# Kernel tuning notes

Measured on AMD Instinct MI355X. Metric: run time of the kernel, lower is better.

The kernel has to match this reference:

```python
import jax, jax.numpy as jnp
import numpy as np

H = 4096          # hidden_size
I = 2048          # moe_intermediate_size * n_shared_experts
SWIGLU_LIMIT = 10.0
QMAX = 127.0


def _quantize_weight(w):
    # per-output-channel symmetric int8 quantization of a float weight [out, in]
    s = jnp.maximum(jnp.max(jnp.abs(w), axis=1) / QMAX, 1e-8)      # [out]
    q = jnp.clip(jnp.round(w / s[:, None]), -QMAX, QMAX)           # int8-valued
    return q.astype(jnp.float32), s.astype(jnp.float32)


def setup_inputs() -> dict:
    key = jax.random.key(0)
    ks = jax.random.split(key, 4)
    x = jax.random.normal(ks[0], (2, 4096, H), dtype=jnp.float32)
    w_gate, s_wgate = _quantize_weight(jax.random.normal(ks[1], (I, H)) * 0.02)
    w_up, s_wup = _quantize_weight(jax.random.normal(ks[2], (I, H)) * 0.02)
    w_down, s_wdown = _quantize_weight(jax.random.normal(ks[3], (H, I)) * 0.02)
    inv_gate = jnp.ones((H,), jnp.float32)
    inv_up = jnp.ones((H,), jnp.float32)
    inv_inter = jnp.ones((I,), jnp.float32)
    return {"x": x, "w_gate": w_gate, "s_wgate": s_wgate, "w_up": w_up,
            "s_wup": s_wup, "w_down": w_down, "s_wdown": s_wdown,
            "inv_gate": inv_gate, "inv_up": inv_up, "inv_inter": inv_inter}


def _dynamic_quant(x, inv_smooth):
    # per-token symmetric int8 dynamic quant with smoothing scale
    xs = x.astype(jnp.float32) * inv_smooth                        # [T, D]
    scale = jnp.maximum(jnp.max(jnp.abs(xs), axis=-1, keepdims=True) / QMAX, 1e-8)
    q = jnp.clip(jnp.round(xs / scale), -QMAX, QMAX)
    return q, scale


def _quant_gemm(q, x_scale, w_q, w_scale):
    acc = q @ w_q.T                                                # fp32 accumulate
    return acc * x_scale * w_scale[None, :]


def reference(x, w_gate, s_wgate, w_up, s_wup, w_down, s_wdown,
              inv_gate, inv_up, inv_inter):
    orig_shape = x.shape
    x_flat = x.reshape(-1, H).astype(jnp.bfloat16)                 # [T, H]
    qg, sg = _dynamic_quant(x_flat, inv_gate)
    qu, su = _dynamic_quant(x_flat, inv_up)
    gate_out = _quant_gemm(qg, sg, w_gate, s_wgate)                # [T, I]
    up_out = _quant_gemm(qu, su, w_up, s_wup)                      # [T, I]
    inter = jax.nn.silu(gate_out) * up_out
    inter = jnp.clip(inter, -SWIGLU_LIMIT, SWIGLU_LIMIT).astype(jnp.bfloat16)
    qi, si = _dynamic_quant(inter, inv_inter)
    out = _quant_gemm(qi, si, w_down, s_wdown)                     # [T, H]
    return out.reshape(orig_shape)
```

## Files before the change

### kernel.cpp

```cpp
#include <hip/hip_runtime.h>
#include <hip/hip_bf16.h>


typedef __attribute__((ext_vector_type(4))) int i32x4;
typedef __attribute__((ext_vector_type(16))) int i32x16;

__device__ __forceinline__ void async16(void* lds, const void* g) {
  __builtin_amdgcn_global_load_lds(
      (const __attribute__((address_space(1))) void*)g,
      (__attribute__((address_space(3))) void*)lds, 16, 0, 0);
}

__device__ __forceinline__ i32x16 mfma32(i32x4 a, i32x4 b, i32x16 c) {
  return __builtin_amdgcn_mfma_i32_32x32x32_i8(a, b, c, 0, 0, 0);
}

__device__ __forceinline__ float bf16_rne_f(float f) {
  unsigned u = __float_as_uint(f);
  u += 0x7fffu + ((u >> 16) & 1u);
  return __uint_as_float(u & 0xffff0000u);
}
__device__ __forceinline__ unsigned short bf16_bits(float f) {
  unsigned u = __float_as_uint(f);
  u += 0x7fffu + ((u >> 16) & 1u);
  return (unsigned short)(u >> 16);
}
__device__ __forceinline__ float bf16_to_f(unsigned short h) {
  return __uint_as_float(((unsigned)h) << 16);
}

__global__ void wconv3_kernel(const float* __restrict__ w0,
                              const float* __restrict__ w1,
                              const float* __restrict__ w2,
                              signed char* __restrict__ q0,
                              signed char* __restrict__ q1,
                              signed char* __restrict__ q2, int n) {
  const float* w = (blockIdx.y == 0) ? w0 : (blockIdx.y == 1) ? w1 : w2;
  signed char* q = (blockIdx.y == 0) ? q0 : (blockIdx.y == 1) ? q1 : q2;
  int i = (blockIdx.x * 256 + threadIdx.x) * 4;
  if (i >= n) return;
  float4 f = *(const float4*)(w + i);
  signed char c[4] __attribute__((aligned(4)));
  c[0] = (signed char)(int)rintf(f.x);
  c[1] = (signed char)(int)rintf(f.y);
  c[2] = (signed char)(int)rintf(f.z);
  c[3] = (signed char)(int)rintf(f.w);
  *(int*)(q + i) = *(const int*)c;
}

__global__ __launch_bounds__(256) void quant_x_kernel(
    const float* __restrict__ x, const float* __restrict__ invg,
    const float* __restrict__ invu, signed char* __restrict__ qg,
    signed char* __restrict__ qu, float* __restrict__ sg,
    float* __restrict__ su, int H) {
  const int t = blockIdx.x, tid = threadIdx.x;
  const float* xr = x + (size_t)t * H;
  const int c0 = tid * 16;
  float xg[16], xu[16];
  float mg = 0.f, mu = 0.f;
#pragma unroll
  for (int v = 0; v < 4; ++v) {
    float4 f = *(const float4*)(xr + c0 + v * 4);
    float4 ig = *(const float4*)(invg + c0 + v * 4);
    float4 iu = *(const float4*)(invu + c0 + v * 4);
    float b0 = bf16_rne_f(f.x), b1 = bf16_rne_f(f.y);
    float b2 = bf16_rne_f(f.z), b3 = bf16_rne_f(f.w);
    xg[v * 4 + 0] = b0 * ig.x; xg[v * 4 + 1] = b1 * ig.y;
    xg[v * 4 + 2] = b2 * ig.z; xg[v * 4 + 3] = b3 * ig.w;
    xu[v * 4 + 0] = b0 * iu.x; xu[v * 4 + 1] = b1 * iu.y;
    xu[v * 4 + 2] = b2 * iu.z; xu[v * 4 + 3] = b3 * iu.w;
#pragma unroll
    for (int j = 0; j < 4; ++j) {
      mg = fmaxf(mg, fabsf(xg[v * 4 + j]));
      mu = fmaxf(mu, fabsf(xu[v * 4 + j]));
    }
  }
#pragma unroll
  for (int off = 32; off > 0; off >>= 1) {
    mg = fmaxf(mg, __shfl_xor(mg, off));
    mu = fmaxf(mu, __shfl_xor(mu, off));
  }
  __shared__ float smg[4], smu[4];
  if ((tid & 63) == 0) { smg[tid >> 6] = mg; smu[tid >> 6] = mu; }
  __syncthreads();
  mg = fmaxf(fmaxf(smg[0], smg[1]), fmaxf(smg[2], smg[3]));
  mu = fmaxf(fmaxf(smu[0], smu[1]), fmaxf(smu[2], smu[3]));
  const float scg = fmaxf(mg / 127.0f, 1e-8f);
  const float scu = fmaxf(mu / 127.0f, 1e-8f);
  const float rg = 1.0f / scg, ru = 1.0f / scu;
  signed char og[16] __attribute__((aligned(16)));
  signed char ou[16] __attribute__((aligned(16)));
#pragma unroll
  for (int j = 0; j < 16; ++j) {
    og[j] = (signed char)(int)fminf(fmaxf(rintf(xg[j] * rg), -127.f), 127.f);
    ou[j] = (signed char)(int)fminf(fmaxf(rintf(xu[j] * ru), -127.f), 127.f);
  }
  *(i32x4*)(qg + (size_t)t * H + c0) = *(const i32x4*)og;
  *(i32x4*)(qu + (size_t)t * H + c0) = *(const i32x4*)ou;
  if (tid == 0) { sg[t] = scg; su[t] = scu; }
}

__global__ __launch_bounds__(256, 2) void gemm1_kernel(
    const signed char* __restrict__ qg, const signed char* __restrict__ qu,
    const float* __restrict__ sg, const float* __restrict__ su,
    const signed char* __restrict__ wg, const signed char* __restrict__ wu,
    const float* __restrict__ swg, const float* __restrict__ swu,
    unsigned short* __restrict__ inter, int H, int I) {
  __shared__ signed char Ag[128 * 64] __attribute__((aligned(16)));
  __shared__ signed char Au[128 * 64] __attribute__((aligned(16)));
  __shared__ signed char Bg[128 * 64] __attribute__((aligned(16)));
  __shared__ signed char Bu[128 * 64] __attribute__((aligned(16)));
  const int tid = threadIdx.x;
  const int lane = tid & 63, wave = tid >> 6;
  const int col0 = blockIdx.x * 128, row0 = blockIdx.y * 128;
  const int wm = (wave & 1) * 64, wn = (wave >> 1) * 64;
  const int m = lane & 31, h = lane >> 5;

  i32x16 accG[2][2], accU[2][2];
#pragma unroll
  for (int i = 0; i < 2; ++i)
#pragma unroll
    for (int j = 0; j < 2; ++j) {
      accG[i][j] = (i32x16)(0);
      accU[i][j] = (i32x16)(0);
    }

  for (int kk = 0; kk < H; kk += 64) {
    __syncthreads();
#pragma unroll
    for (int p = 0; p < 2; ++p) {
      const int g = p * 256 + tid;
      const int r = g >> 2;
      const int cg = ((g & 3) - r) & 3;
      const size_t ga = (size_t)(row0 + r) * H + kk + cg * 16;
      const size_t gb = (size_t)(col0 + r) * H + kk + cg * 16;
      async16(&Ag[g * 16], qg + ga);
      async16(&Au[g * 16], qu + ga);
      async16(&Bg[g * 16], wg + gb);
      async16(&Bu[g * 16], wu + gb);
    }
    __syncthreads();
#pragma unroll
    for (int s = 0; s < 2; ++s) {
      i32x4 aG[2], aU[2], bG[2], bU[2];
#pragma unroll
      for (int i = 0; i < 2; ++i) {
        const int ra = wm + i * 32 + m;
        const int ca = ((s * 2 + h + ra) & 3) * 16;
        aG[i] = *(const i32x4*)&Ag[ra * 64 + ca];
        aU[i] = *(const i32x4*)&Au[ra * 64 + ca];
        const int rb = wn + i * 32 + m;
        const int cb = ((s * 2 + h + rb) & 3) * 16;
        bG[i] = *(const i32x4*)&Bg[rb * 64 + cb];
        bU[i] = *(const i32x4*)&Bu[rb * 64 + cb];
      }
#pragma unroll
      for (int i = 0; i < 2; ++i)
#pragma unroll
        for (int j = 0; j < 2; ++j) {
          accG[i][j] = mfma32(aG[i], bG[j], accG[i][j]);
          accU[i][j] = mfma32(aU[i], bU[j], accU[i][j]);
        }
    }
  }

  float swgc[2], swuc[2];
#pragma unroll
  for (int j = 0; j < 2; ++j) {
    const int c = col0 + wn + j * 32 + m;
    swgc[j] = swg[c];
    swuc[j] = swu[c];
  }
#pragma unroll
  for (int i = 0; i < 2; ++i) {
#pragma unroll
    for (int reg = 0; reg < 16; ++reg) {
      const int row = row0 + wm + i * 32 + (reg & 3) + 8 * (reg >> 2) + 4 * h;
      const float sgr = sg[row], sur = su[row];
#pragma unroll
      for (int j = 0; j < 2; ++j) {
        const int c = col0 + wn + j * 32 + m;
        const float g = (float)accG[i][j][reg] * sgr * swgc[j];
        const float u = (float)accU[i][j][reg] * sur * swuc[j];
        const float sig = 1.f / (1.f + __expf(-g));
        float v = (g * sig) * u;
        v = fminf(fmaxf(v, -10.f), 10.f);
        inter[(size_t)row * I + c] = bf16_bits(v);
      }
    }
  }
}

__global__ __launch_bounds__(256) void quant_i_kernel(
    const unsigned short* __restrict__ inter, const float* __restrict__ invi,
    signed char* __restrict__ qi, float* __restrict__ si, int I) {
  const int t = blockIdx.x, tid = threadIdx.x;
  const unsigned short* ir = inter + (size_t)t * I;
  const int c0 = tid * 8;
  uint4 pk = *(const uint4*)(ir + c0);
  float4 i0 = *(const float4*)(invi + c0);
  float4 i1 = *(const float4*)(invi + c0 + 4);
  float xs[8];
  xs[0] = bf16_to_f(pk.x & 0xffffu) * i0.x;
  xs[1] = bf16_to_f(pk.x >> 16) * i0.y;
  xs[2] = bf16_to_f(pk.y & 0xffffu) * i0.z;
  xs[3] = bf16_to_f(pk.y >> 16) * i0.w;
  xs[4] = bf16_to_f(pk.z & 0xffffu) * i1.x;
  xs[5] = bf16_to_f(pk.z >> 16) * i1.y;
  xs[6] = bf16_to_f(pk.w & 0xffffu) * i1.z;
  xs[7] = bf16_to_f(pk.w >> 16) * i1.w;
  float m = 0.f;
#pragma unroll
  for (int j = 0; j < 8; ++j) m = fmaxf(m, fabsf(xs[j]));
#pragma unroll
  for (int off = 32; off > 0; off >>= 1) m = fmaxf(m, __shfl_xor(m, off));
  __shared__ float sm[4];
  if ((tid & 63) == 0) sm[tid >> 6] = m;
  __syncthreads();
  m = fmaxf(fmaxf(sm[0], sm[1]), fmaxf(sm[2], sm[3]));
  const float s = fmaxf(m / 127.0f, 1e-8f);
  const float rs = 1.0f / s;
  signed char o[8] __attribute__((aligned(8)));
#pragma unroll
  for (int j = 0; j < 8; ++j)
    o[j] = (signed char)(int)fminf(fmaxf(rintf(xs[j] * rs), -127.f), 127.f);
  *(unsigned long long*)(qi + (size_t)t * I + c0) = *(const unsigned long long*)o;
  if (tid == 0) si[t] = s;
}

__global__ __launch_bounds__(256, 2) void gemm2_kernel(
    const signed char* __restrict__ qi, const float* __restrict__ si,
    const signed char* __restrict__ wd, const float* __restrict__ swd,
    float* __restrict__ out, int H, int I) {
  __shared__ signed char As[128 * 64] __attribute__((aligned(16)));
  __shared__ signed char Bs[128 * 64] __attribute__((aligned(16)));
  const int tid = threadIdx.x;
  const int lane = tid & 63, wave = tid >> 6;
  const int col0 = blockIdx.x * 128, row0 = blockIdx.y * 128;
  const int wm = (wave & 1) * 64, wn = (wave >> 1) * 64;
  const int m = lane & 31, h = lane >> 5;

  i32x16 acc[2][2];
#pragma unroll
  for (int i = 0; i < 2; ++i)
#pragma unroll
    for (int j = 0; j < 2; ++j) acc[i][j] = (i32x16)(0);

  for (int kk = 0; kk < I; kk += 64) {
    __syncthreads();
#pragma unroll
    for (int p = 0; p < 2; ++p) {
      const int g = p * 256 + tid;
      const int r = g >> 2;
      const int cg = ((g & 3) - r) & 3;
      async16(&As[g * 16], qi + (size_t)(row0 + r) * I + kk + cg * 16);
      async16(&Bs[g * 16], wd + (size_t)(col0 + r) * I + kk + cg * 16);
    }
    __syncthreads();
#pragma unroll
    for (int s = 0; s < 2; ++s) {
      i32x4 a[2], b[2];
#pragma unroll
      for (int i = 0; i < 2; ++i) {
        const int ra = wm + i * 32 + m;
        const int ca = ((s * 2 + h + ra) & 3) * 16;
        a[i] = *(const i32x4*)&As[ra * 64 + ca];
        const int rb = wn + i * 32 + m;
        const int cb = ((s * 2 + h + rb) & 3) * 16;
        b[i] = *(const i32x4*)&Bs[rb * 64 + cb];
      }
#pragma unroll
      for (int i = 0; i < 2; ++i)
#pragma unroll
        for (int j = 0; j < 2; ++j) acc[i][j] = mfma32(a[i], b[j], acc[i][j]);
    }
  }

  float swc[2];
#pragma unroll
  for (int j = 0; j < 2; ++j) swc[j] = swd[col0 + wn + j * 32 + m];
#pragma unroll
  for (int i = 0; i < 2; ++i) {
#pragma unroll
    for (int reg = 0; reg < 16; ++reg) {
      const int row = row0 + wm + i * 32 + (reg & 3) + 8 * (reg >> 2) + 4 * h;
      const float sir = si[row];
#pragma unroll
      for (int j = 0; j < 2; ++j) {
        const int c = col0 + wn + j * 32 + m;
        out[(size_t)row * H + c] = (float)acc[i][j][reg] * sir * swc[j];
      }
    }
  }
}

extern "C" void kernel_launch(void* const* d_in, const int* in_sizes, int n_in,
                              void* d_out, int out_size, void* d_ws,
                              size_t ws_size, hipStream_t stream) {
  const float* x = (const float*)d_in[0];
  const float* w_gate = (const float*)d_in[1];
  const float* s_wgate = (const float*)d_in[2];
  const float* w_up = (const float*)d_in[3];
  const float* s_wup = (const float*)d_in[4];
  const float* w_down = (const float*)d_in[5];
  const float* s_wdown = (const float*)d_in[6];
  const float* inv_gate = (const float*)d_in[7];
  const float* inv_up = (const float*)d_in[8];
  const float* inv_inter = (const float*)d_in[9];
  float* out = (float*)d_out;

  const int H = in_sizes[6];
  const int I = in_sizes[2];
  const int T = in_sizes[0] / H;

  char* ws = (char*)d_ws;
  size_t off = 0;
  signed char* wqg = (signed char*)(ws + off); off += (size_t)I * H;
  signed char* wqu = (signed char*)(ws + off); off += (size_t)I * H;
  signed char* wqd = (signed char*)(ws + off); off += (size_t)H * I;
  signed char* qg  = (signed char*)(ws + off); off += (size_t)T * H;
  signed char* qu  = (signed char*)(ws + off); off += (size_t)T * H;
  unsigned short* inter = (unsigned short*)(ws + off); off += (size_t)T * I * 2;
  float* sg = (float*)(ws + off); off += (size_t)T * 4;
  float* su = (float*)(ws + off); off += (size_t)T * 4;
  float* si = (float*)(ws + off); off += (size_t)T * 4;
  signed char* qi = qg;

  const int nW = I * H;
  dim3 gw(nW / 1024, 3);
  wconv3_kernel<<<gw, 256, 0, stream>>>(w_gate, w_up, w_down, wqg, wqu, wqd, nW);

  quant_x_kernel<<<T, 256, 0, stream>>>(x, inv_gate, inv_up, qg, qu, sg, su, H);

  dim3 g1(I / 128, T / 128);
  gemm1_kernel<<<g1, 256, 0, stream>>>(qg, qu, sg, su, wqg, wqu, s_wgate,
                                       s_wup, inter, H, I);

  quant_i_kernel<<<T, 256, 0, stream>>>(inter, inv_inter, qi, si, I);

  dim3 g2(H / 128, T / 128);
  gemm2_kernel<<<g2, 256, 0, stream>>>(qi, si, wqd, s_wdown, out, H, I);
}
```

Baseline: 608.2 us.

## Pre-tile int8 operands into MFMA-native blocked layout for contiguous tile loads

The weight conversion and both activation quant kernels now write int8 data in a blocked layout (32-row tiles, 16-byte k-chunks arranged per MFMA fragment). The GEMMs can then fetch each k-tile with contiguous 16-byte async loads and read LDS fragments at fixed offsets, with no swizzle arithmetic. The grid order is swapped so row blocks vary fastest, and quant_i now handles two tokens per block. In exchange, the weight conversion writes strided output, and the layout only works when T, H and I are multiples of 32 and 64.

```diff
diff --git a/kernel.cpp b/kernel.cpp
--- a/kernel.cpp
+++ b/kernel.cpp
@@ -29,23 +29,36 @@
   return __uint_as_float(((unsigned)h) << 16);
 }
 
-__global__ void wconv3_kernel(const float* __restrict__ w0,
-                              const float* __restrict__ w1,
-                              const float* __restrict__ w2,
-                              signed char* __restrict__ q0,
-                              signed char* __restrict__ q1,
-                              signed char* __restrict__ q2, int n) {
-  const float* w = (blockIdx.y == 0) ? w0 : (blockIdx.y == 1) ? w1 : w2;
-  signed char* q = (blockIdx.y == 0) ? q0 : (blockIdx.y == 1) ? q1 : q2;
-  int i = (blockIdx.x * 256 + threadIdx.x) * 4;
-  if (i >= n) return;
-  float4 f = *(const float4*)(w + i);
-  signed char c[4] __attribute__((aligned(4)));
-  c[0] = (signed char)(int)rintf(f.x);
-  c[1] = (signed char)(int)rintf(f.y);
-  c[2] = (signed char)(int)rintf(f.z);
-  c[3] = (signed char)(int)rintf(f.w);
-  *(int*)(q + i) = *(const int*)c;
+__global__ __launch_bounds__(256) void wconv_kernel(
+    const float* __restrict__ w0, const float* __restrict__ w1,
+    const float* __restrict__ w2, signed char* __restrict__ q0,
+    signed char* __restrict__ q1, signed char* __restrict__ q2,
+    int H, int I) {
+  const int wid = blockIdx.y;
+  const float* w = (wid == 0) ? w0 : (wid == 1) ? w1 : w2;
+  signed char* q = (wid == 0) ? q0 : (wid == 1) ? q1 : q2;
+  const int K = (wid == 2) ? I : H;
+  const int R = (wid == 2) ? H : I;
+  const int rt = blockIdx.x;
+  if (rt * 32 >= R) return;
+  const int m = threadIdx.x & 31, sub = threadIdx.x >> 5;
+  const int row = rt * 32 + m;
+  const int nkc = K >> 4;
+  const size_t outTile = (size_t)rt * K * 32 + (size_t)m * 16;
+  for (int kc = sub; kc < nkc; kc += 8) {
+    const float* src = w + (size_t)row * K + kc * 16;
+    signed char c[16] __attribute__((aligned(16)));
+#pragma unroll
+    for (int v = 0; v < 4; ++v) {
+      float4 f = *(const float4*)(src + v * 4);
+      c[v * 4 + 0] = (signed char)(int)rintf(f.x);
+      c[v * 4 + 1] = (signed char)(int)rintf(f.y);
+      c[v * 4 + 2] = (signed char)(int)rintf(f.z);
+      c[v * 4 + 3] = (signed char)(int)rintf(f.w);
+    }
+    *(i32x4*)(q + outTile + (kc >> 2) * 2048 + (kc & 3) * 512) =
+        *(const i32x4*)c;
+  }
 }
 
 __global__ __launch_bounds__(256) void quant_x_kernel(
@@ -95,8 +108,10 @@
     og[j] = (signed char)(int)fminf(fmaxf(rintf(xg[j] * rg), -127.f), 127.f);
     ou[j] = (signed char)(int)fminf(fmaxf(rintf(xu[j] * ru), -127.f), 127.f);
   }
-  *(i32x4*)(qg + (size_t)t * H + c0) = *(const i32x4*)og;
-  *(i32x4*)(qu + (size_t)t * H + c0) = *(const i32x4*)ou;
+  const size_t off8 = (size_t)(t >> 5) * H * 32 + (tid >> 2) * 2048 +
+                      (tid & 3) * 512 + (t & 31) * 16;
+  *(i32x4*)(qg + off8) = *(const i32x4*)og;
+  *(i32x4*)(qu + off8) = *(const i32x4*)ou;
   if (tid == 0) { sg[t] = scg; su[t] = scu; }
 }
 
@@ -112,9 +127,20 @@
   __shared__ signed char Bu[128 * 64] __attribute__((aligned(16)));
   const int tid = threadIdx.x;
   const int lane = tid & 63, wave = tid >> 6;
-  const int col0 = blockIdx.x * 128, row0 = blockIdx.y * 128;
-  const int wm = (wave & 1) * 64, wn = (wave >> 1) * 64;
+  const int row0 = blockIdx.x * 128, col0 = blockIdx.y * 128;
+  const int ah = wave & 1, bh = wave >> 1;
   const int m = lane & 31, h = lane >> 5;
+
+  const size_t rts = (size_t)H * 32;
+  const int o = tid & 127, mt0 = tid >> 7;
+  const size_t aoff = (size_t)(row0 >> 5) * rts + (size_t)mt0 * rts + o * 16;
+  const size_t boff = (size_t)(col0 >> 5) * rts + (size_t)mt0 * rts + o * 16;
+  const signed char* pAg = qg + aoff;
+  const signed char* pAu = qu + aoff;
+  const signed char* pBg = wg + boff;
+  const signed char* pBu = wu + boff;
+  const int lds0 = tid * 16, lds1 = tid * 16 + 4096;
+  const size_t skip = rts * 2;
 
   i32x16 accG[2][2], accU[2][2];
 #pragma unroll
@@ -125,34 +151,32 @@
       accU[i][j] = (i32x16)(0);
     }
 
-  for (int kk = 0; kk < H; kk += 64) {
+  const signed char* aBaseG = &Ag[ah * 4096 + lane * 16];
+  const signed char* aBaseU = &Au[ah * 4096 + lane * 16];
+  const signed char* bBaseG = &Bg[bh * 4096 + lane * 16];
+  const signed char* bBaseU = &Bu[bh * 4096 + lane * 16];
+
+  for (int kt = 0; kt < (H >> 6); ++kt) {
     __syncthreads();
-#pragma unroll
-    for (int p = 0; p < 2; ++p) {
-      const int g = p * 256 + tid;
-      const int r = g >> 2;
-      const int cg = ((g & 3) - r) & 3;
-      const size_t ga = (size_t)(row0 + r) * H + kk + cg * 16;
-      const size_t gb = (size_t)(col0 + r) * H + kk + cg * 16;
-      async16(&Ag[g * 16], qg + ga);
-      async16(&Au[g * 16], qu + ga);
-      async16(&Bg[g * 16], wg + gb);
-      async16(&Bu[g * 16], wu + gb);
-    }
+    async16(&Ag[lds0], pAg);
+    async16(&Ag[lds1], pAg + skip);
+    async16(&Au[lds0], pAu);
+    async16(&Au[lds1], pAu + skip);
+    async16(&Bg[lds0], pBg);
+    async16(&Bg[lds1], pBg + skip);
+    async16(&Bu[lds0], pBu);
+    async16(&Bu[lds1], pBu + skip);
+    pAg += 2048; pAu += 2048; pBg += 2048; pBu += 2048;
     __syncthreads();
 #pragma unroll
     for (int s = 0; s < 2; ++s) {
       i32x4 aG[2], aU[2], bG[2], bU[2];
 #pragma unroll
       for (int i = 0; i < 2; ++i) {
-        const int ra = wm + i * 32 + m;
-        const int ca = ((s * 2 + h + ra) & 3) * 16;
-        aG[i] = *(const i32x4*)&Ag[ra * 64 + ca];
-        aU[i] = *(const i32x4*)&Au[ra * 64 + ca];
-        const int rb = wn + i * 32 + m;
-        const int cb = ((s * 2 + h + rb) & 3) * 16;
-        bG[i] = *(const i32x4*)&Bg[rb * 64 + cb];
-        bU[i] = *(const i32x4*)&Bu[rb * 64 + cb];
+        aG[i] = *(const i32x4*)(aBaseG + i * 2048 + s * 1024);
+        aU[i] = *(const i32x4*)(aBaseU + i * 2048 + s * 1024);
+        bG[i] = *(const i32x4*)(bBaseG + i * 2048 + s * 1024);
+        bU[i] = *(const i32x4*)(bBaseU + i * 2048 + s * 1024);
       }
 #pragma unroll
       for (int i = 0; i < 2; ++i)
@@ -167,7 +191,7 @@
   float swgc[2], swuc[2];
 #pragma unroll
   for (int j = 0; j < 2; ++j) {
-    const int c = col0 + wn + j * 32 + m;
+    const int c = col0 + bh * 64 + j * 32 + m;
     swgc[j] = swg[c];
     swuc[j] = swu[c];
   }
@@ -175,11 +199,12 @@
   for (int i = 0; i < 2; ++i) {
 #pragma unroll
     for (int reg = 0; reg < 16; ++reg) {
-      const int row = row0 + wm + i * 32 + (reg & 3) + 8 * (reg >> 2) + 4 * h;
+      const int row =
+          row0 + ah * 64 + i * 32 + (reg & 3) + 8 * (reg >> 2) + 4 * h;
       const float sgr = sg[row], sur = su[row];
 #pragma unroll
       for (int j = 0; j < 2; ++j) {
-        const int c = col0 + wn + j * 32 + m;
+        const int c = col0 + bh * 64 + j * 32 + m;
         const float g = (float)accG[i][j][reg] * sgr * swgc[j];
         const float u = (float)accU[i][j][reg] * sur * swuc[j];
         const float sig = 1.f / (1.f + __expf(-g));
@@ -194,38 +219,41 @@
 __global__ __launch_bounds__(256) void quant_i_kernel(
     const unsigned short* __restrict__ inter, const float* __restrict__ invi,
     signed char* __restrict__ qi, float* __restrict__ si, int I) {
-  const int t = blockIdx.x, tid = threadIdx.x;
-  const unsigned short* ir = inter + (size_t)t * I;
-  const int c0 = tid * 8;
-  uint4 pk = *(const uint4*)(ir + c0);
-  float4 i0 = *(const float4*)(invi + c0);
-  float4 i1 = *(const float4*)(invi + c0 + 4);
-  float xs[8];
-  xs[0] = bf16_to_f(pk.x & 0xffffu) * i0.x;
-  xs[1] = bf16_to_f(pk.x >> 16) * i0.y;
-  xs[2] = bf16_to_f(pk.y & 0xffffu) * i0.z;
-  xs[3] = bf16_to_f(pk.y >> 16) * i0.w;
-  xs[4] = bf16_to_f(pk.z & 0xffffu) * i1.x;
-  xs[5] = bf16_to_f(pk.z >> 16) * i1.y;
-  xs[6] = bf16_to_f(pk.w & 0xffffu) * i1.z;
-  xs[7] = bf16_to_f(pk.w >> 16) * i1.w;
-  float m = 0.f;
-#pragma unroll
-  for (int j = 0; j < 8; ++j) m = fmaxf(m, fabsf(xs[j]));
-#pragma unroll
-  for (int off = 32; off > 0; off >>= 1) m = fmaxf(m, __shfl_xor(m, off));
+  const int tid = threadIdx.x;
+  const int t = blockIdx.x * 2 + (tid >> 7);
+  const int kc = tid & 127;
+  const unsigned short* ir = inter + (size_t)t * I + kc * 16;
+  uint4 p0 = *(const uint4*)ir;
+  uint4 p1 = *(const uint4*)(ir + 8);
+  const float* iv = invi + kc * 16;
+  float xs[16];
+  {
+    const unsigned pk[8] = {p0.x, p0.y, p0.z, p0.w, p1.x, p1.y, p1.z, p1.w};
+#pragma unroll
+    for (int j = 0; j < 8; ++j) {
+      xs[j * 2] = bf16_to_f((unsigned short)(pk[j] & 0xffffu)) * iv[j * 2];
+      xs[j * 2 + 1] = bf16_to_f((unsigned short)(pk[j] >> 16)) * iv[j * 2 + 1];
+    }
+  }
+  float mx = 0.f;
+#pragma unroll
+  for (int j = 0; j < 16; ++j) mx = fmaxf(mx, fabsf(xs[j]));
+#pragma unroll
+  for (int off = 32; off > 0; off >>= 1) mx = fmaxf(mx, __shfl_xor(mx, off));
   __shared__ float sm[4];
-  if ((tid & 63) == 0) sm[tid >> 6] = m;
+  if ((tid & 63) == 0) sm[tid >> 6] = mx;
   __syncthreads();
-  m = fmaxf(fmaxf(sm[0], sm[1]), fmaxf(sm[2], sm[3]));
-  const float s = fmaxf(m / 127.0f, 1e-8f);
+  mx = (tid >> 7) ? fmaxf(sm[2], sm[3]) : fmaxf(sm[0], sm[1]);
+  const float s = fmaxf(mx / 127.0f, 1e-8f);
   const float rs = 1.0f / s;
-  signed char o[8] __attribute__((aligned(8)));
-#pragma unroll
-  for (int j = 0; j < 8; ++j)
-    o[j] = (signed char)(int)fminf(fmaxf(rintf(xs[j] * rs), -127.f), 127.f);
-  *(unsigned long long*)(qi + (size_t)t * I + c0) = *(const unsigned long long*)o;
-  if (tid == 0) si[t] = s;
+  signed char oq[16] __attribute__((aligned(16)));
+#pragma unroll
+  for (int j = 0; j < 16; ++j)
+    oq[j] = (signed char)(int)fminf(fmaxf(rintf(xs[j] * rs), -127.f), 127.f);
+  const size_t off8 = (size_t)(t >> 5) * I * 32 + (kc >> 2) * 2048 +
+                      (kc & 3) * 512 + (t & 31) * 16;
+  *(i32x4*)(qi + off8) = *(const i32x4*)oq;
+  if (kc == 0) si[t] = s;
 }
 
 __global__ __launch_bounds__(256, 2) void gemm2_kernel(
@@ -236,38 +264,43 @@
   __shared__ signed char Bs[128 * 64] __attribute__((aligned(16)));
   const int tid = threadIdx.x;
   const int lane = tid & 63, wave = tid >> 6;
-  const int col0 = blockIdx.x * 128, row0 = blockIdx.y * 128;
-  const int wm = (wave & 1) * 64, wn = (wave >> 1) * 64;
+  const int row0 = blockIdx.x * 128, col0 = blockIdx.y * 128;
+  const int ah = wave & 1, bh = wave >> 1;
   const int m = lane & 31, h = lane >> 5;
 
+  const size_t rts = (size_t)I * 32;
+  const int o = tid & 127, mt0 = tid >> 7;
+  const signed char* pA =
+      qi + (size_t)(row0 >> 5) * rts + (size_t)mt0 * rts + o * 16;
+  const signed char* pB =
+      wd + (size_t)(col0 >> 5) * rts + (size_t)mt0 * rts + o * 16;
+  const int lds0 = tid * 16, lds1 = tid * 16 + 4096;
+  const size_t skip = rts * 2;
+
   i32x16 acc[2][2];
 #pragma unroll
   for (int i = 0; i < 2; ++i)
 #pragma unroll
     for (int j = 0; j < 2; ++j) acc[i][j] = (i32x16)(0);
 
-  for (int kk = 0; kk < I; kk += 64) {
+  const signed char* aBase = &As[ah * 4096 + lane * 16];
+  const signed char* bBase = &Bs[bh * 4096 + lane * 16];
+
+  for (int kt = 0; kt < (I >> 6); ++kt) {
     __syncthreads();
-#pragma unroll
-    for (int p = 0; p < 2; ++p) {
-      const int g = p * 256 + tid;
-      const int r = g >> 2;
-      const int cg = ((g & 3) - r) & 3;
-      async16(&As[g * 16], qi + (size_t)(row0 + r) * I + kk + cg * 16);
-      async16(&Bs[g * 16], wd + (size_t)(col0 + r) * I + kk + cg * 16);
-    }
+    async16(&As[lds0], pA);
+    async16(&As[lds1], pA + skip);
+    async16(&Bs[lds0], pB);
+    async16(&Bs[lds1], pB + skip);
+    pA += 2048; pB += 2048;
     __syncthreads();
 #pragma unroll
     for (int s = 0; s < 2; ++s) {
       i32x4 a[2], b[2];
 #pragma unroll
       for (int i = 0; i < 2; ++i) {
-        const int ra = wm + i * 32 + m;
-        const int ca = ((s * 2 + h + ra) & 3) * 16;
-        a[i] = *(const i32x4*)&As[ra * 64 + ca];
-        const int rb = wn + i * 32 + m;
-        const int cb = ((s * 2 + h + rb) & 3) * 16;
-        b[i] = *(const i32x4*)&Bs[rb * 64 + cb];
+        a[i] = *(const i32x4*)(aBase + i * 2048 + s * 1024);
+        b[i] = *(const i32x4*)(bBase + i * 2048 + s * 1024);
       }
 #pragma unroll
       for (int i = 0; i < 2; ++i)
@@ -278,16 +311,17 @@
 
   float swc[2];
 #pragma unroll
-  for (int j = 0; j < 2; ++j) swc[j] = swd[col0 + wn + j * 32 + m];
+  for (int j = 0; j < 2; ++j) swc[j] = swd[col0 + bh * 64 + j * 32 + m];
 #pragma unroll
   for (int i = 0; i < 2; ++i) {
 #pragma unroll
     for (int reg = 0; reg < 16; ++reg) {
-      const int row = row0 + wm + i * 32 + (reg & 3) + 8 * (reg >> 2) + 4 * h;
+      const int row =
+          row0 + ah * 64 + i * 32 + (reg & 3) + 8 * (reg >> 2) + 4 * h;
       const float sir = si[row];
 #pragma unroll
       for (int j = 0; j < 2; ++j) {
-        const int c = col0 + wn + j * 32 + m;
+        const int c = col0 + bh * 64 + j * 32 + m;
         out[(size_t)row * H + c] = (float)acc[i][j][reg] * sir * swc[j];
       }
     }
@@ -326,18 +360,18 @@
   float* si = (float*)(ws + off); off += (size_t)T * 4;
   signed char* qi = qg;
 
-  const int nW = I * H;
-  dim3 gw(nW / 1024, 3);
-  wconv3_kernel<<<gw, 256, 0, stream>>>(w_gate, w_up, w_down, wqg, wqu, wqd, nW);
+  dim3 gw(H / 32, 3);
+  wconv_kernel<<<gw, 256, 0, stream>>>(w_gate, w_up, w_down, wqg, wqu, wqd,
+                                       H, I);
 
   quant_x_kernel<<<T, 256, 0, stream>>>(x, inv_gate, inv_up, qg, qu, sg, su, H);
 
-  dim3 g1(I / 128, T / 128);
+  dim3 g1(T / 128, I / 128);
   gemm1_kernel<<<g1, 256, 0, stream>>>(qg, qu, sg, su, wqg, wqu, s_wgate,
                                        s_wup, inter, H, I);
 
-  quant_i_kernel<<<T, 256, 0, stream>>>(inter, inv_inter, qi, si, I);
-
-  dim3 g2(H / 128, T / 128);
+  quant_i_kernel<<<T / 2, 256, 0, stream>>>(inter, inv_inter, qi, si, I);
+
+  dim3 g2(T / 128, H / 128);
   gemm2_kernel<<<g2, 256, 0, stream>>>(qi, si, wqd, s_wdown, out, H, I);
 }
```

Result: no change. 620.2 us (+2.0%).
